# Optimization experiments

Hardware: AMD Instinct MI355X
Metric: run time of the kernel (lower is better)

Reference implementation:

```python
import math
import jax, jax.numpy as jnp
import numpy as np

NB_HEADS = 32
NB_KV_HEADS = 8
HEAD_DIM = 64
ROPE_THETA = 10000.0


def _rope_modulator(seq_len, dim, theta):
    # (seq_len, dim//2, 2): (cos, sin) of 2*pi*t / theta^(2k/d)  -- note nonstandard 2*pi factor
    freqs = 1.0 / theta ** (jnp.arange(0, dim - 1, 2, dtype=jnp.float32) / dim)
    t = jnp.arange(seq_len, dtype=jnp.float32) * (2.0 * math.pi)
    angles = t[:, None] * freqs[None, :]
    return jnp.stack((jnp.cos(angles), jnp.sin(angles)), axis=-1)


def _apply_rope(qk, rm):
    # qk: (B, H, S, hd); pairs are consecutive (even, odd) lanes
    B, H, S, hd = qk.shape
    qk = qk.reshape(B, H, S, hd // 2, 2)
    c, s = rm[:S, :, 0], rm[:S, :, 1]  # (S, hd//2)
    re = qk[..., 0] * c - qk[..., 1] * s
    im = qk[..., 0] * s + qk[..., 1] * c
    return jnp.stack((re, im), axis=-1).reshape(B, H, S, hd)


def setup_inputs() -> dict:
    key = jax.random.key(0)
    k1, k2, k3, k4, k5 = jax.random.split(key, 5)
    D = NB_HEADS * HEAD_DIM  # 2048
    Dkv = NB_KV_HEADS * HEAD_DIM  # 512
    std = D ** -0.5
    return {
        "x": jax.random.normal(k1, (2, 2048, D), dtype=jnp.float32),
        "Wq": jax.random.normal(k2, (D, D), dtype=jnp.float32) * std,
        "Wk": jax.random.normal(k3, (Dkv, D), dtype=jnp.float32) * std,
        "Wv": jax.random.normal(k4, (Dkv, D), dtype=jnp.float32) * std,
        "Wo": jax.random.normal(k5, (D, D), dtype=jnp.float32) * std,
    }


def reference(x, Wq, Wk, Wv, Wo):
    B, S, D = x.shape
    g = NB_HEADS // NB_KV_HEADS
    rm = _rope_modulator(S, HEAD_DIM, ROPE_THETA)

    q = (x @ Wq.T).reshape(B, S, NB_HEADS, HEAD_DIM).transpose(0, 2, 1, 3)
    k = (x @ Wk.T).reshape(B, S, NB_KV_HEADS, HEAD_DIM).transpose(0, 2, 1, 3)
    v = (x @ Wv.T).reshape(B, S, NB_KV_HEADS, HEAD_DIM).transpose(0, 2, 1, 3)

    q = _apply_rope(q, rm)
    k = _apply_rope(k, rm)

    # GQA: expand KV heads (repeat_interleave over head dim)
    k = jnp.repeat(k, g, axis=1)  # (B, H, S, hd)
    v = jnp.repeat(v, g, axis=1)

    scale = 1.0 / math.sqrt(HEAD_DIM)
    scores = jnp.einsum("bhqd,bhkd->bhqk", q, k) * scale
    causal = jnp.tril(jnp.ones((S, S), dtype=bool))
    scores = jnp.where(causal, scores, jnp.finfo(scores.dtype).min)
    attn = jax.nn.softmax(scores, axis=-1)
    z = jnp.einsum("bhqk,bhkd->bhqd", attn, v)  # (B, H, S, hd)
    z = z.transpose(0, 2, 1, 3).reshape(B, S, D)
    return z @ Wo.T
```

## Files before the change

### kernel.cpp

```cpp
#include <hip/hip_runtime.h>
#include <hip/hip_bf16.h>
#include <math.h>

#define B_   2
#define S_   2048
#define H_   32
#define HKV_ 8
#define HD_  64
#define D_   2048
#define DKV_ 512
#define M_   (B_*S_)

typedef __attribute__((ext_vector_type(8))) short bf16x8;
typedef __attribute__((ext_vector_type(4))) float f32x4;
typedef __attribute__((ext_vector_type(16))) float f32x16;
typedef unsigned short u16;

__device__ __forceinline__ u16 f2bf(float f) {
    union { float f; unsigned u; } v; v.f = f;
    unsigned r = v.u + 0x7fff + ((v.u >> 16) & 1);
    return (u16)(r >> 16);
}

__device__ __forceinline__ unsigned cvt_pk_bf16(float lo, float hi) {
    unsigned r;
    asm("v_cvt_pk_bf16_f32 %0, %1, %2" : "=v"(r) : "v"(lo), "v"(hi));
    return r;
}
__device__ __forceinline__ void perm32swap(unsigned &a, unsigned &b) {
    asm volatile("v_permlane32_swap_b32 %0, %1" : "+v"(a), "+v"(b));
}

typedef __attribute__((address_space(3))) void lds_void;
typedef const __attribute__((address_space(1))) void g_void;
__device__ __forceinline__ void gl_lds16(const void* g, void* l) {
    __builtin_amdgcn_global_load_lds((g_void*)g, (lds_void*)l, 16, 0, 0);
}

__global__ void rope_table_kernel(float* __restrict__ tab) {
    int idx = blockIdx.x * blockDim.x + threadIdx.x;
    int s = idx >> 5, i = idx & 31;
    double freq = pow(10000.0, -(double)i / 32.0);
    double ang = (double)s * 6.283185307179586476925286766559 * freq;
    tab[2*idx]   = (float)cos(ang);
    tab[2*idx+1] = (float)sin(ang);
}

__global__ void cvt_all_kernel(const float* __restrict__ x,  const float* __restrict__ wq,
                               const float* __restrict__ wk, const float* __restrict__ wv,
                               u16* __restrict__ xb, u16* __restrict__ wall) {
    int i = blockIdx.x * blockDim.x + threadIdx.x;
    if (i >= 1835008) return;
    const float* src; u16* dst;
    size_t e = (size_t)i * 8;
    if (i < 1048576)      { src = x  + e;            dst = xb + e; }
    else if (i < 1572864) { src = wq + (e - 8388608);  dst = wall + (e - 8388608); }
    else if (i < 1703936) { src = wk + (e - 12582912); dst = wall + 4194304 + (e - 12582912); }
    else                  { src = wv + (e - 13631488); dst = wall + 5242880 + (e - 13631488); }
    float4 a = *(const float4*)src;
    float4 b = *(const float4*)(src + 4);
    u16 tmp[8] = {f2bf(a.x), f2bf(a.y), f2bf(a.z), f2bf(a.w),
                  f2bf(b.x), f2bf(b.y), f2bf(b.z), f2bf(b.w)};
    *(uint4*)dst = *(const uint4*)tmp;
}

__global__ void cvt_bf16_kernel(const float* __restrict__ src, u16* __restrict__ dst, int n8) {
    int i = blockIdx.x * blockDim.x + threadIdx.x;
    if (i >= n8) return;
    const float4* p = (const float4*)(src + (size_t)i * 8);
    float4 a = p[0], b = p[1];
    u16 tmp[8] = {f2bf(a.x), f2bf(a.y), f2bf(a.z), f2bf(a.w),
                  f2bf(b.x), f2bf(b.y), f2bf(b.z), f2bf(b.w)};
    *(uint4*)(dst + (size_t)i * 8) = *(const uint4*)tmp;
}

template<bool YF32, bool ROPE>
__launch_bounds__(256, 2)
__global__ void gemm_bt_bf16(const u16* __restrict__ X, const u16* __restrict__ W,
                             void* __restrict__ Y, const float2* __restrict__ tab,
                             int Ndim, int Kdim) {
    __shared__ u16 As[128*32];
    __shared__ u16 Bs[128*32];
    int tid = threadIdx.x;
    int wv = tid >> 6, lane = tid & 63;
    int quad = lane >> 4, lr = lane & 15;
    int wm = wv >> 1, wn = wv & 1;
    int m0 = blockIdx.y * 128, n0 = blockIdx.x * 128;

    int srow = wv*32 + (lane >> 2);
    int scol = (lane & 3) * 8;
    const u16* xp = X + (size_t)(m0 + srow)*Kdim + scol;
    const u16* wp = W + (size_t)(n0 + srow)*Kdim + scol;

    f32x4 acc[4][4] = {};
    for (int k0 = 0; k0 < Kdim; k0 += 32) {
        __syncthreads();
        gl_lds16(xp + k0,                   &As[wv*1024]);
        gl_lds16(xp + 16*(size_t)Kdim + k0, &As[wv*1024 + 512]);
        gl_lds16(wp + k0,                   &Bs[wv*1024]);
        gl_lds16(wp + 16*(size_t)Kdim + k0, &Bs[wv*1024 + 512]);
        __syncthreads();
        bf16x8 af[4], bfr[4];
        #pragma unroll
        for (int t = 0; t < 4; ++t) {
            af[t]  = *(const bf16x8*)(&As[(wm*64 + t*16 + lr)*32 + quad*8]);
            bfr[t] = *(const bf16x8*)(&Bs[(wn*64 + t*16 + lr)*32 + quad*8]);
        }
        #pragma unroll
        for (int mt = 0; mt < 4; ++mt)
            #pragma unroll
            for (int nt = 0; nt < 4; ++nt)
                acc[mt][nt] = __builtin_amdgcn_mfma_f32_16x16x32_bf16(af[mt], bfr[nt], acc[mt][nt], 0, 0, 0);
    }
    #pragma unroll
    for (int mt = 0; mt < 4; ++mt)
        #pragma unroll
        for (int nt = 0; nt < 4; ++nt)
            #pragma unroll
            for (int r = 0; r < 4; ++r) {
                int m = m0 + wm*64 + mt*16 + quad*4 + r;
                int n = n0 + wn*64 + nt*16 + lr;
                float val = acc[mt][nt][r];
                if constexpr (ROPE) {
                    float partner = __shfl_xor(val, 1);
                    if (n < 2560) {
                        float2 cs = tab[(size_t)(m & (S_-1))*32 + ((n >> 1) & 31)];
                        val = fmaf(cs.x, val, ((n & 1) ? cs.y : -cs.y) * partner);
                    }
                }
                if constexpr (YF32)
                    ((float*)Y)[(size_t)m*Ndim + n] = val;
                else
                    ((u16*)Y)[(size_t)m*Ndim + n] = f2bf(val);
            }
}

#define LDK 40
template<bool F32>
__device__ __forceinline__ void stage8(const void* src, u16* dst, size_t row, int col, int ld) {
    if constexpr (F32) {
        const float* p = (const float*)src + row * (size_t)ld + col;
        float4 a = *(const float4*)p;
        float4 b = *(const float4*)(p + 4);
        u16 tmp[8] = {f2bf(a.x), f2bf(a.y), f2bf(a.z), f2bf(a.w),
                      f2bf(b.x), f2bf(b.y), f2bf(b.z), f2bf(b.w)};
        *(uint4*)dst = *(const uint4*)tmp;
    } else {
        const u16* p = (const u16*)src + row * (size_t)ld + col;
        *(uint4*)dst = *(const uint4*)p;
    }
}

template<bool XF32, bool WF32, bool YF32, bool ROPE>
__launch_bounds__(256, 2)
__global__ void gemm_bt(const void* __restrict__ X, const void* __restrict__ W,
                        void* __restrict__ Y, const float2* __restrict__ tab,
                        int Ndim, int Kdim) {
    __shared__ u16 As[128*LDK];
    __shared__ u16 Bs[128*LDK];
    int tid = threadIdx.x;
    int wv = tid >> 6, lane = tid & 63;
    int quad = lane >> 4, lr = lane & 15;
    int wm = wv >> 1, wn = wv & 1;
    int m0 = blockIdx.y * 128, n0 = blockIdx.x * 128;

    f32x4 acc[4][4] = {};
    for (int k0 = 0; k0 < Kdim; k0 += 32) {
        __syncthreads();
        #pragma unroll
        for (int it = 0; it < 2; ++it) {
            int e = (it*256 + tid) * 8;
            int r = e >> 5, kk = e & 31;
            stage8<XF32>(X, &As[r*LDK + kk], (size_t)(m0 + r), k0 + kk, Kdim);
            stage8<WF32>(W, &Bs[r*LDK + kk], (size_t)(n0 + r), k0 + kk, Kdim);
        }
        __syncthreads();
        bf16x8 af[4], bfr[4];
        #pragma unroll
        for (int t = 0; t < 4; ++t) {
            af[t]  = *(const bf16x8*)(&As[(wm*64 + t*16 + lr)*LDK + quad*8]);
            bfr[t] = *(const bf16x8*)(&Bs[(wn*64 + t*16 + lr)*LDK + quad*8]);
        }
        #pragma unroll
        for (int mt = 0; mt < 4; ++mt)
            #pragma unroll
            for (int nt = 0; nt < 4; ++nt)
                acc[mt][nt] = __builtin_amdgcn_mfma_f32_16x16x32_bf16(af[mt], bfr[nt], acc[mt][nt], 0, 0, 0);
    }
    #pragma unroll
    for (int mt = 0; mt < 4; ++mt)
        #pragma unroll
        for (int nt = 0; nt < 4; ++nt)
            #pragma unroll
            for (int r = 0; r < 4; ++r) {
                int m = m0 + wm*64 + mt*16 + quad*4 + r;
                int n = n0 + wn*64 + nt*16 + lr;
                float val = acc[mt][nt][r];
                if constexpr (ROPE) {
                    float partner = __shfl_xor(val, 1);
                    if (n < 2560) {
                        float2 cs = tab[(size_t)(m & (S_-1))*32 + ((n >> 1) & 31)];
                        val = fmaf(cs.x, val, ((n & 1) ? cs.y : -cs.y) * partner);
                    }
                }
                if constexpr (YF32)
                    ((float*)Y)[(size_t)m*Ndim + n] = val;
                else
                    ((u16*)Y)[(size_t)m*Ndim + n] = f2bf(val);
            }
}

__launch_bounds__(256, 4)
__global__ void attn_kernel(const u16* __restrict__ qkv, u16* __restrict__ z) {
    __shared__ u16 Ks[2][64*64];
    __shared__ u16 Vt[2][64*64];
    int tid = threadIdx.x;
    int wv = tid >> 6, lane = tid & 63;
    int qcol = lane & 31, hi = lane >> 5;
    int id = blockIdx.x;
    int qt = 15 - (id >> 6);
    int bh = id & 63;
    int h = bh >> 1, b = bh & 1;
    int kvh = h >> 2;
    int qrow_base = qt*128 + wv*32;
    int jmax = 2*qt + 1;

    const u16* qkvb = qkv + (size_t)(b*S_) * 3072;
    const u16* kbase = qkvb + 2048 + kvh*64;

    int kr = lane >> 3;
    int dcs = lane & 7;
    int sg = tid & 7;
    int sp = tid >> 3;
    const u16* vbase = qkvb + 2560 + kvh*64 + sg*8;

    #pragma unroll
    for (int i = 0; i < 2; ++i) {
        int c = 2*wv + i;
        int kvloc = c*8 + kr;
        int dc = dcs ^ ((kvloc + (kvloc >> 3)) & 7);
        gl_lds16(kbase + (size_t)kvloc*3072 + dc*8, &Ks[0][c*512]);
    }
    uint4 vr0 = *(const uint4*)(vbase + (size_t)(2*sp)*3072);
    uint4 vr1 = *(const uint4*)(vbase + (size_t)(2*sp + 1)*3072);

    bf16x8 bq[4];
    {
        const u16* qp = qkvb + (size_t)(qrow_base + qcol)*3072 + h*64 + hi*8;
        #pragma unroll
        for (int ds = 0; ds < 4; ++ds)
            bq[ds] = *(const bf16x8*)(qp + ds*16);
    }

    f32x16 oacc[2] = {};
    float lsum = 0.f;
    const float SC = 0.18033688f;

    for (int j = 0; j <= jmax; ++j) {
        int buf = j & 1;
        {
            const u16* a0 = (const u16*)&vr0;
            const u16* a1 = (const u16*)&vr1;
            #pragma unroll
            for (int jx = 0; jx < 8; ++jx) {
                unsigned pk = (unsigned)a0[jx] | ((unsigned)a1[jx] << 16);
                int kvs = (2*sp) ^ (8*(jx ^ sg));
                *(unsigned*)(&Vt[buf][(sg*8 + jx)*64 + kvs]) = pk;
            }
        }
        __syncthreads();

        if (j < jmax) {
            int kvn = (j+1)*64;
            #pragma unroll
            for (int i = 0; i < 2; ++i) {
                int c = 2*wv + i;
                int kvloc = c*8 + kr;
                int dc = dcs ^ ((kvloc + (kvloc >> 3)) & 7);
                gl_lds16(kbase + (size_t)(kvn + kvloc)*3072 + dc*8, &Ks[buf^1][c*512]);
            }
            vr0 = *(const uint4*)(vbase + (size_t)(kvn + 2*sp)*3072);
            vr1 = *(const uint4*)(vbase + (size_t)(kvn + 2*sp + 1)*3072);
        }

        int kv0 = j*64;
        if (kv0 < qrow_base + 32) {
            #pragma unroll
            for (int t = 0; t < 2; ++t) {
                int kvt = kv0 + t*32;
                if (kvt <= qrow_base + 31) {
                    f32x16 sacc = {};
                    int krow = t*32 + qcol;
                    int ksw = (krow + (krow >> 3)) & 7;
                    #pragma unroll
                    for (int ds = 0; ds < 4; ++ds) {
                        bf16x8 ak = *(const bf16x8*)(&Ks[buf][krow*64 + (((2*ds + hi) ^ ksw)*8)]);
                        sacc = __builtin_amdgcn_mfma_f32_32x32x16_bf16(ak, bq[ds], sacc, 0, 0, 0);
                    }
                    float p[16];
                    if (kvt + 31 > qrow_base) {
                        #pragma unroll
                        for (int r = 0; r < 16; ++r) {
                            int kvg = kvt + (r & 3) + 8*(r >> 2) + 4*hi;
                            float pv = exp2f(fmaf(sacc[r], SC, -4.0f));
                            if (kvg > qrow_base + qcol) pv = 0.f;
                            p[r] = pv; lsum += pv;
                        }
                    } else {
                        #pragma unroll
                        for (int r = 0; r < 16; ++r) {
                            p[r] = exp2f(fmaf(sacc[r], SC, -4.0f));
                            lsum += p[r];
                        }
                    }
                    unsigned U0[4], U1[4];
                    #pragma unroll
                    for (int g = 0; g < 4; ++g) {
                        U0[g] = cvt_pk_bf16(p[4*g],     p[4*g + 1]);
                        U1[g] = cvt_pk_bf16(p[4*g + 2], p[4*g + 3]);
                    }
                    #pragma unroll
                    for (int s = 0; s < 2; ++s) {
                        unsigned w0 = U0[2*s], w2 = U0[2*s + 1];
                        unsigned w1 = U1[2*s], w3 = U1[2*s + 1];
                        perm32swap(w0, w2);
                        perm32swap(w1, w3);
                        uint4 paw; paw.x = w0; paw.y = w1; paw.z = w2; paw.w = w3;
                        bf16x8 pa = __builtin_bit_cast(bf16x8, paw);
                        #pragma unroll
                        for (int dt = 0; dt < 2; ++dt) {
                            int d = dt*32 + qcol;
                            int g8 = (d & 7) ^ ((d >> 3) & 7);
                            int lc = 4*t + 2*s + hi;
                            bf16x8 bv = *(const bf16x8*)(&Vt[buf][d*64 + ((lc ^ g8)*8)]);
                            oacc[dt] = __builtin_amdgcn_mfma_f32_32x32x16_bf16(pa, bv, oacc[dt], 0, 0, 0);
                        }
                    }
                }
            }
        }
    }

    lsum += __shfl_xor(lsum, 32);
    __syncthreads();
    float* Lb = (float*)&Ks[0][0];
    if (hi == 0) Lb[wv*32 + qcol] = lsum;
    __syncthreads();

    #pragma unroll
    for (int r = 0; r < 16; ++r) {
        int crow = (r & 3) + 8*(r >> 2) + 4*hi;
        int row = qrow_base + crow;
        float li = Lb[wv*32 + crow];
        #pragma unroll
        for (int dt = 0; dt < 2; ++dt)
            z[(size_t)(b*S_ + row)*D_ + h*64 + dt*32 + qcol] = f2bf(oacc[dt][r] / li);
    }
}

extern "C" void kernel_launch(void* const* d_in, const int* in_sizes, int n_in,
                              void* d_out, int out_size, void* d_ws, size_t ws_size,
                              hipStream_t stream) {
    const float* x  = (const float*)d_in[0];
    const float* Wq = (const float*)d_in[1];
    const float* Wk = (const float*)d_in[2];
    const float* Wv = (const float*)d_in[3];
    const float* Wo = (const float*)d_in[4];
    float* out = (float*)d_out;
    char* ws = (char*)d_ws;

    const size_t OFF_XB   = 0;
    const size_t OFF_WALL = 16777216;
    const size_t OFF_TAB  = 29360128;
    const size_t OFF_QKV  = 29884416;
    const size_t NEED     = 55050240;

    float*  tab  = (float*)(ws + OFF_TAB);
    float2* tab2 = (float2*)(ws + OFF_TAB);

    if (ws_size >= NEED) {
        u16* xb   = (u16*)(ws + OFF_XB);
        u16* wall = (u16*)(ws + OFF_WALL);
        u16* qkv  = (u16*)(ws + OFF_QKV);
        u16* zbuf = (u16*)(ws + OFF_XB);
        u16* wob  = (u16*)(ws + 16777216);

        rope_table_kernel<<<256, 256, 0, stream>>>(tab);
        cvt_all_kernel<<<7168, 256, 0, stream>>>(x, Wq, Wk, Wv, xb, wall);
        gemm_bt_bf16<false, true><<<dim3(24, 32), 256, 0, stream>>>(xb, wall, qkv, tab2, 3072, 2048);
        cvt_bf16_kernel<<<2048, 256, 0, stream>>>(Wo, wob, D_*D_/8);
        attn_kernel<<<1024, 256, 0, stream>>>(qkv, zbuf);
        gemm_bt_bf16<true, false><<<dim3(16, 32), 256, 0, stream>>>(zbuf, wob, out, tab2, 2048, 2048);
    } else {
        u16* qkv  = (u16*)(ws + 524288);
        u16* zbuf = (u16*)(ws + 524288 + (size_t)M_*3072*2);

        rope_table_kernel<<<256, 256, 0, stream>>>(tab);
        gemm_bt<true, true, false, true ><<<dim3(16, 32), 256, 0, stream>>>(x, Wq, qkv,        tab2, 3072, 2048);
        gemm_bt<true, true, false, true ><<<dim3(4,  32), 256, 0, stream>>>(x, Wk, qkv + 2048, tab2, 3072, 2048);
        gemm_bt<true, true, false, false><<<dim3(4,  32), 256, 0, stream>>>(x, Wv, qkv + 2560, tab2, 3072, 2048);
        attn_kernel<<<1024, 256, 0, stream>>>(qkv, zbuf);
        gemm_bt<false, true, true, false><<<dim3(16, 32), 256, 0, stream>>>(zbuf, Wo, out, tab2, 2048, 2048);
    }
}
```

Measured before the change: 301.9 us.

## Use 256x256 GEMM tiles with triple-buffered async LDS pipeline

Replaces the 128x128 bf16 GEMM with a 256x256-tile, 512-thread kernel that prefetches three K-slices into LDS ahead of time. It uses explicit vmcnt waits and single barriers, so global loads overlap with the MFMA work. It also raises MFMA priority during compute. The larger tiles improve data reuse, but the grid shrinks to 192 and 128 blocks, which may underfill the 256 CUs, and triple buffering uses 96KB of LDS per block.

Measured after the change: 359.9 us. 1.19x slower.

```diff
diff --git a/kernel.cpp b/kernel.cpp
--- a/kernel.cpp
+++ b/kernel.cpp
@@ -75,50 +75,82 @@
 }
 
 template<bool YF32, bool ROPE>
-__launch_bounds__(256, 2)
-__global__ void gemm_bt_bf16(const u16* __restrict__ X, const u16* __restrict__ W,
-                             void* __restrict__ Y, const float2* __restrict__ tab,
-                             int Ndim, int Kdim) {
-    __shared__ u16 As[128*32];
-    __shared__ u16 Bs[128*32];
+__launch_bounds__(512, 2)
+__global__ void gemm_bt_256(const u16* __restrict__ X, const u16* __restrict__ W,
+                            void* __restrict__ Y, const float2* __restrict__ tab,
+                            int Ndim, int Kdim) {
+    __shared__ u16 As[3][256*32];
+    __shared__ u16 Bs[3][256*32];
     int tid = threadIdx.x;
-    int wv = tid >> 6, lane = tid & 63;
+    int wvid = tid >> 6, lane = tid & 63;
     int quad = lane >> 4, lr = lane & 15;
-    int wm = wv >> 1, wn = wv & 1;
-    int m0 = blockIdx.y * 128, n0 = blockIdx.x * 128;
-
-    int srow = wv*32 + (lane >> 2);
-    int scol = (lane & 3) * 8;
-    const u16* xp = X + (size_t)(m0 + srow)*Kdim + scol;
-    const u16* wp = W + (size_t)(n0 + srow)*Kdim + scol;
-
-    f32x4 acc[4][4] = {};
-    for (int k0 = 0; k0 < Kdim; k0 += 32) {
-        __syncthreads();
-        gl_lds16(xp + k0,                   &As[wv*1024]);
-        gl_lds16(xp + 16*(size_t)Kdim + k0, &As[wv*1024 + 512]);
-        gl_lds16(wp + k0,                   &Bs[wv*1024]);
-        gl_lds16(wp + 16*(size_t)Kdim + k0, &Bs[wv*1024 + 512]);
-        __syncthreads();
-        bf16x8 af[4], bfr[4];
-        #pragma unroll
-        for (int t = 0; t < 4; ++t) {
-            af[t]  = *(const bf16x8*)(&As[(wm*64 + t*16 + lr)*32 + quad*8]);
-            bfr[t] = *(const bf16x8*)(&Bs[(wn*64 + t*16 + lr)*32 + quad*8]);
-        }
-        #pragma unroll
-        for (int mt = 0; mt < 4; ++mt)
+    int wm = wvid >> 2, wn = wvid & 3;
+    int m0 = blockIdx.y * 256, n0 = blockIdx.x * 256;
+    const u16* Xb = X + (size_t)m0 * Kdim;
+    const u16* Wb = W + (size_t)n0 * Kdim;
+
+    int rsub = lane >> 2;
+    int cch  = (lane & 3) * 8;
+    int r0   = wvid * 32;
+    int NT   = Kdim >> 5;
+
+    #pragma unroll
+    for (int tt = 0; tt < 3; ++tt) {
+        int k0 = tt * 32;
+        #pragma unroll
+        for (int i = 0; i < 2; ++i) {
+            int br = r0 + i*16;
+            gl_lds16(Xb + (size_t)(br + rsub)*Kdim + k0 + cch, &As[tt][br*32]);
+            gl_lds16(Wb + (size_t)(br + rsub)*Kdim + k0 + cch, &Bs[tt][br*32]);
+        }
+    }
+    asm volatile("s_waitcnt vmcnt(8)" ::: "memory");
+    __builtin_amdgcn_s_barrier();
+
+    f32x4 acc[8][4] = {};
+    int slot = 0;
+    for (int t = 0; t < NT; ++t) {
+        bf16x8 af[8], bfr[4];
+        const u16* as = &As[slot][0];
+        const u16* bs = &Bs[slot][0];
+        #pragma unroll
+        for (int mt = 0; mt < 8; ++mt)
+            af[mt] = *(const bf16x8*)(as + (wm*128 + mt*16 + lr)*32 + quad*8);
+        #pragma unroll
+        for (int nt = 0; nt < 4; ++nt)
+            bfr[nt] = *(const bf16x8*)(bs + (wn*64 + nt*16 + lr)*32 + quad*8);
+        asm volatile("s_waitcnt lgkmcnt(0)" ::: "memory");
+        __builtin_amdgcn_s_barrier();
+        if (t + 3 < NT) {
+            int k0 = (t + 3) * 32;
+            #pragma unroll
+            for (int i = 0; i < 2; ++i) {
+                int br = r0 + i*16;
+                gl_lds16(Xb + (size_t)(br + rsub)*Kdim + k0 + cch, &As[slot][br*32]);
+                gl_lds16(Wb + (size_t)(br + rsub)*Kdim + k0 + cch, &Bs[slot][br*32]);
+            }
+        }
+        __builtin_amdgcn_s_setprio(1);
+        #pragma unroll
+        for (int mt = 0; mt < 8; ++mt)
             #pragma unroll
             for (int nt = 0; nt < 4; ++nt)
                 acc[mt][nt] = __builtin_amdgcn_mfma_f32_16x16x32_bf16(af[mt], bfr[nt], acc[mt][nt], 0, 0, 0);
-    }
+        __builtin_amdgcn_s_setprio(0);
+        if (t + 3 < NT)      asm volatile("s_waitcnt vmcnt(8)" ::: "memory");
+        else if (t + 2 < NT) asm volatile("s_waitcnt vmcnt(4)" ::: "memory");
+        else if (t + 1 < NT) asm volatile("s_waitcnt vmcnt(0)" ::: "memory");
+        __builtin_amdgcn_s_barrier();
+        slot = (slot == 2) ? 0 : slot + 1;
+    }
+
     #pragma unroll
-    for (int mt = 0; mt < 4; ++mt)
+    for (int mt = 0; mt < 8; ++mt)
         #pragma unroll
         for (int nt = 0; nt < 4; ++nt)
             #pragma unroll
             for (int r = 0; r < 4; ++r) {
-                int m = m0 + wm*64 + mt*16 + quad*4 + r;
+                int m = m0 + wm*128 + mt*16 + quad*4 + r;
                 int n = n0 + wn*64 + nt*16 + lr;
                 float val = acc[mt][nt][r];
                 if constexpr (ROPE) {
@@ -387,10 +419,10 @@
 
         rope_table_kernel<<<256, 256, 0, stream>>>(tab);
         cvt_all_kernel<<<7168, 256, 0, stream>>>(x, Wq, Wk, Wv, xb, wall);
-        gemm_bt_bf16<false, true><<<dim3(24, 32), 256, 0, stream>>>(xb, wall, qkv, tab2, 3072, 2048);
+        gemm_bt_256<false, true><<<dim3(12, 16), 512, 0, stream>>>(xb, wall, qkv, tab2, 3072, 2048);
         cvt_bf16_kernel<<<2048, 256, 0, stream>>>(Wo, wob, D_*D_/8);
         attn_kernel<<<1024, 256, 0, stream>>>(qkv, zbuf);
-        gemm_bt_bf16<true, false><<<dim3(16, 32), 256, 0, stream>>>(zbuf, wob, out, tab2, 2048, 2048);
+        gemm_bt_256<true, false><<<dim3(8, 16), 512, 0, stream>>>(zbuf, wob, out, tab2, 2048, 2048);
     } else {
         u16* qkv  = (u16*)(ws + 524288);
         u16* zbuf = (u16*)(ws + 524288 + (size_t)M_*3072*2);
```

## Triple-buffer bf16 GEMM LDS tiles with async prefetch and register double-buffering

Applied to the files above, without the earlier changes.

Replaces the single-buffered bf16 GEMM main loop with a three-stage LDS ring, issuing global-to-LDS loads three K-tiles ahead and waiting only on vmcnt for the oldest tile. It also preloads the next tile's fragments into registers while the MFMAs for the current tile run, and raises wave priority around the MFMA block. The aim is to hide global load latency and reduce barrier stalls in the QKV and output projections. LDS use triples, and launch bounds are raised to 3 blocks per CU, which adds register pressure and risks spills.

New measurement: 312.9 us. 3.6% more time.

```diff
diff --git a/kernel.cpp b/kernel.cpp
--- a/kernel.cpp
+++ b/kernel.cpp
@@ -75,12 +75,12 @@
 }
 
 template<bool YF32, bool ROPE>
-__launch_bounds__(256, 2)
-__global__ void gemm_bt_bf16(const u16* __restrict__ X, const u16* __restrict__ W,
-                             void* __restrict__ Y, const float2* __restrict__ tab,
-                             int Ndim, int Kdim) {
-    __shared__ u16 As[128*32];
-    __shared__ u16 Bs[128*32];
+__launch_bounds__(256, 3)
+__global__ void gemm_bt_p(const u16* __restrict__ X, const u16* __restrict__ W,
+                          void* __restrict__ Y, const float2* __restrict__ tab,
+                          int Ndim, int Kdim) {
+    __shared__ u16 As[3][128*32];
+    __shared__ u16 Bs[3][128*32];
     int tid = threadIdx.x;
     int wv = tid >> 6, lane = tid & 63;
     int quad = lane >> 4, lr = lane & 15;
@@ -91,27 +91,62 @@
     int scol = (lane & 3) * 8;
     const u16* xp = X + (size_t)(m0 + srow)*Kdim + scol;
     const u16* wp = W + (size_t)(n0 + srow)*Kdim + scol;
+    int NT = Kdim >> 5;
+
+    #pragma unroll
+    for (int tt = 0; tt < 3; ++tt) {
+        int k0 = tt << 5;
+        gl_lds16(xp + k0,                   &As[tt][wv*1024]);
+        gl_lds16(xp + 16*(size_t)Kdim + k0, &As[tt][wv*1024 + 512]);
+        gl_lds16(wp + k0,                   &Bs[tt][wv*1024]);
+        gl_lds16(wp + 16*(size_t)Kdim + k0, &Bs[tt][wv*1024 + 512]);
+    }
+    asm volatile("s_waitcnt vmcnt(8)" ::: "memory");
+    __builtin_amdgcn_s_barrier();
+
+    bf16x8 af[4], bfr[4], nf[4], nb[4];
+    #pragma unroll
+    for (int t4 = 0; t4 < 4; ++t4) {
+        af[t4]  = *(const bf16x8*)(&As[0][(wm*64 + t4*16 + lr)*32 + quad*8]);
+        bfr[t4] = *(const bf16x8*)(&Bs[0][(wn*64 + t4*16 + lr)*32 + quad*8]);
+    }
 
     f32x4 acc[4][4] = {};
-    for (int k0 = 0; k0 < Kdim; k0 += 32) {
-        __syncthreads();
-        gl_lds16(xp + k0,                   &As[wv*1024]);
-        gl_lds16(xp + 16*(size_t)Kdim + k0, &As[wv*1024 + 512]);
-        gl_lds16(wp + k0,                   &Bs[wv*1024]);
-        gl_lds16(wp + 16*(size_t)Kdim + k0, &Bs[wv*1024 + 512]);
-        __syncthreads();
-        bf16x8 af[4], bfr[4];
-        #pragma unroll
-        for (int t = 0; t < 4; ++t) {
-            af[t]  = *(const bf16x8*)(&As[(wm*64 + t*16 + lr)*32 + quad*8]);
-            bfr[t] = *(const bf16x8*)(&Bs[(wn*64 + t*16 + lr)*32 + quad*8]);
-        }
+    int slot = 0;
+    for (int t = 0; t < NT; ++t) {
+        asm volatile("s_waitcnt lgkmcnt(0)" ::: "memory");
+        __builtin_amdgcn_s_barrier();
+        if (t + 3 < NT) {
+            int k0 = (t + 3) << 5;
+            gl_lds16(xp + k0,                   &As[slot][wv*1024]);
+            gl_lds16(xp + 16*(size_t)Kdim + k0, &As[slot][wv*1024 + 512]);
+            gl_lds16(wp + k0,                   &Bs[slot][wv*1024]);
+            gl_lds16(wp + 16*(size_t)Kdim + k0, &Bs[slot][wv*1024 + 512]);
+        }
+        int slot1 = (slot == 2) ? 0 : slot + 1;
+        if (t + 1 < NT) {
+            if (t + 3 < NT)      asm volatile("s_waitcnt vmcnt(8)" ::: "memory");
+            else if (t + 2 < NT) asm volatile("s_waitcnt vmcnt(4)" ::: "memory");
+            else                 asm volatile("s_waitcnt vmcnt(0)" ::: "memory");
+            __builtin_amdgcn_s_barrier();
+            #pragma unroll
+            for (int t4 = 0; t4 < 4; ++t4) {
+                nf[t4] = *(const bf16x8*)(&As[slot1][(wm*64 + t4*16 + lr)*32 + quad*8]);
+                nb[t4] = *(const bf16x8*)(&Bs[slot1][(wn*64 + t4*16 + lr)*32 + quad*8]);
+            }
+        }
+        __builtin_amdgcn_s_setprio(1);
         #pragma unroll
         for (int mt = 0; mt < 4; ++mt)
             #pragma unroll
             for (int nt = 0; nt < 4; ++nt)
                 acc[mt][nt] = __builtin_amdgcn_mfma_f32_16x16x32_bf16(af[mt], bfr[nt], acc[mt][nt], 0, 0, 0);
-    }
+        __builtin_amdgcn_s_setprio(0);
+        #pragma unroll
+        for (int t4 = 0; t4 < 4; ++t4) { af[t4] = nf[t4]; bfr[t4] = nb[t4]; }
+        slot = slot1;
+    }
+
     #pragma unroll
     for (int mt = 0; mt < 4; ++mt)
         #pragma unroll
@@ -387,10 +422,10 @@
 
         rope_table_kernel<<<256, 256, 0, stream>>>(tab);
         cvt_all_kernel<<<7168, 256, 0, stream>>>(x, Wq, Wk, Wv, xb, wall);
-        gemm_bt_bf16<false, true><<<dim3(24, 32), 256, 0, stream>>>(xb, wall, qkv, tab2, 3072, 2048);
+        gemm_bt_p<false, true><<<dim3(24, 32), 256, 0, stream>>>(xb, wall, qkv, tab2, 3072, 2048);
         cvt_bf16_kernel<<<2048, 256, 0, stream>>>(Wo, wob, D_*D_/8);
         attn_kernel<<<1024, 256, 0, stream>>>(qkv, zbuf);
-        gemm_bt_bf16<true, false><<<dim3(16, 32), 256, 0, stream>>>(zbuf, wob, out, tab2, 2048, 2048);
+        gemm_bt_p<true, false><<<dim3(16, 32), 256, 0, stream>>>(zbuf, wob, out, tab2, 2048, 2048);
     } else {
         u16* qkv  = (u16*)(ws + 524288);
         u16* zbuf = (u16*)(ws + 524288 + (size_t)M_*3072*2);
```

## Replace bf16 GEMM with 256x256 double-buffered 8-phase pipelined kernel

Applied to the files above, without the earlier changes.

Replaces the 128x128, single-buffered bf16 GEMM with a 256x256 tile kernel using 8 waves and double-buffered LDS. It also XOR-swizzles the LDS layout and splits each K step into four phases. Each phase issues the next tile's global-to-LDS loads while running MFMAs under raised wave priority, with explicit vmcnt waits and barriers. The aim is to hide global load latency, raise data reuse per block and cut LDS bank conflicts. The cost is far fewer blocks (192 and 128) than the GPU has CUs, so part of the chip may sit idle, plus heavy LDS use per block.

Result: slower. 366.7 us (+21.4%).

```diff
diff --git a/kernel.cpp b/kernel.cpp
--- a/kernel.cpp
+++ b/kernel.cpp
@@ -74,51 +74,99 @@
     *(uint4*)(dst + (size_t)i * 8) = *(const uint4*)tmp;
 }
 
+#define GPH(BI, MH, NH, W4, STA, G0, G1, KT) do {                                          \
+    if (W4) asm volatile("s_waitcnt vmcnt(4)" ::: "memory");                               \
+    asm volatile("" ::: "memory");                                                         \
+    __builtin_amdgcn_s_barrier();                                                          \
+    asm volatile("" ::: "memory");                                                         \
+    bf16x8 af_[4][2], bf_[2][2];                                                           \
+    _Pragma("unroll")                                                                      \
+    for (int mtl = 0; mtl < 4; ++mtl)                                                      \
+        _Pragma("unroll")                                                                  \
+        for (int kk = 0; kk < 2; ++kk)                                                     \
+            af_[mtl][kk] = *(const bf16x8*)(&As[BI][(rA + ((MH)*4+mtl)*16)*64 + (((kk*4+quad)^sw)*8)]); \
+    _Pragma("unroll")                                                                      \
+    for (int ntl = 0; ntl < 2; ++ntl)                                                      \
+        _Pragma("unroll")                                                                  \
+        for (int kk = 0; kk < 2; ++kk)                                                     \
+            bf_[ntl][kk] = *(const bf16x8*)(&Bs[BI][(rB + ((NH)*2+ntl)*16)*64 + (((kk*4+quad)^sw)*8)]); \
+    { int k0s_ = (KT) << 6;                                                                \
+      if (STA) { gl_lds16(xsrc + ((size_t)((G0)*8))*Kdim + k0s_, &As[1-(BI)][(G0)*512]);   \
+                 gl_lds16(xsrc + ((size_t)((G1)*8))*Kdim + k0s_, &As[1-(BI)][(G1)*512]); } \
+      else     { gl_lds16(wsrc + ((size_t)((G0)*8))*Kdim + k0s_, &Bs[1-(BI)][(G0)*512]);   \
+                 gl_lds16(wsrc + ((size_t)((G1)*8))*Kdim + k0s_, &Bs[1-(BI)][(G1)*512]); } } \
+    asm volatile("s_waitcnt lgkmcnt(0)" ::: "memory");                                     \
+    __builtin_amdgcn_sched_barrier(0);                                                     \
+    __builtin_amdgcn_s_setprio(1);                                                         \
+    _Pragma("unroll")                                                                      \
+    for (int mtl = 0; mtl < 4; ++mtl)                                                      \
+        _Pragma("unroll")                                                                  \
+        for (int ntl = 0; ntl < 2; ++ntl) {                                                \
+            acc[(MH)*4+mtl][(NH)*2+ntl] = __builtin_amdgcn_mfma_f32_16x16x32_bf16(af_[mtl][0], bf_[ntl][0], acc[(MH)*4+mtl][(NH)*2+ntl], 0, 0, 0); \
+            acc[(MH)*4+mtl][(NH)*2+ntl] = __builtin_amdgcn_mfma_f32_16x16x32_bf16(af_[mtl][1], bf_[ntl][1], acc[(MH)*4+mtl][(NH)*2+ntl], 0, 0, 0); \
+        }                                                                                  \
+    __builtin_amdgcn_s_setprio(0);                                                         \
+} while (0)
+
 template<bool YF32, bool ROPE>
-__launch_bounds__(256, 2)
-__global__ void gemm_bt_bf16(const u16* __restrict__ X, const u16* __restrict__ W,
-                             void* __restrict__ Y, const float2* __restrict__ tab,
-                             int Ndim, int Kdim) {
-    __shared__ u16 As[128*32];
-    __shared__ u16 Bs[128*32];
+__launch_bounds__(512, 2)
+__global__ void gemm_bt_8p(const u16* __restrict__ X, const u16* __restrict__ W,
+                           void* __restrict__ Y, const float2* __restrict__ tab,
+                           int Ndim, int Kdim) {
+    __shared__ u16 As[2][256*64];
+    __shared__ u16 Bs[2][256*64];
     int tid = threadIdx.x;
-    int wv = tid >> 6, lane = tid & 63;
+    int wvid = tid >> 6, lane = tid & 63;
     int quad = lane >> 4, lr = lane & 15;
-    int wm = wv >> 1, wn = wv & 1;
-    int m0 = blockIdx.y * 128, n0 = blockIdx.x * 128;
-
-    int srow = wv*32 + (lane >> 2);
-    int scol = (lane & 3) * 8;
-    const u16* xp = X + (size_t)(m0 + srow)*Kdim + scol;
-    const u16* wp = W + (size_t)(n0 + srow)*Kdim + scol;
-
-    f32x4 acc[4][4] = {};
-    for (int k0 = 0; k0 < Kdim; k0 += 32) {
-        __syncthreads();
-        gl_lds16(xp + k0,                   &As[wv*1024]);
-        gl_lds16(xp + 16*(size_t)Kdim + k0, &As[wv*1024 + 512]);
-        gl_lds16(wp + k0,                   &Bs[wv*1024]);
-        gl_lds16(wp + 16*(size_t)Kdim + k0, &Bs[wv*1024 + 512]);
-        __syncthreads();
-        bf16x8 af[4], bfr[4];
-        #pragma unroll
-        for (int t = 0; t < 4; ++t) {
-            af[t]  = *(const bf16x8*)(&As[(wm*64 + t*16 + lr)*32 + quad*8]);
-            bfr[t] = *(const bf16x8*)(&Bs[(wn*64 + t*16 + lr)*32 + quad*8]);
-        }
-        #pragma unroll
-        for (int mt = 0; mt < 4; ++mt)
-            #pragma unroll
-            for (int nt = 0; nt < 4; ++nt)
-                acc[mt][nt] = __builtin_amdgcn_mfma_f32_16x16x32_bf16(af[mt], bfr[nt], acc[mt][nt], 0, 0, 0);
-    }
+    int wm = wvid >> 2, wn = wvid & 3;
+    int m0 = blockIdx.y * 256, n0 = blockIdx.x * 256;
+    int sw = lr & 7;
+    int rA = wm*128 + lr;
+    int rB = wn*64 + lr;
+
+    int lgr = lane >> 3, lch = lane & 7;
+    size_t goff = (size_t)lgr * Kdim + (size_t)((lch ^ lgr) * 8);
+    const u16* xsrc = X + (size_t)m0 * Kdim + goff;
+    const u16* wsrc = W + (size_t)n0 * Kdim + goff;
+
+    int c0 = wvid*2, c1 = wvid*2 + 1;
+    int gA0 = (c0>>3)*16 + (c0&7),     gA1 = (c1>>3)*16 + (c1&7);
+    int gA2 = (c0>>3)*16 + 8 + (c0&7), gA3 = (c1>>3)*16 + 8 + (c1&7);
+    int gB0 = (c0>>2)*8 + (c0&3),      gB1 = (c1>>2)*8 + (c1&3);
+    int gB2 = (c0>>2)*8 + 4 + (c0&3),  gB3 = (c1>>2)*8 + 4 + (c1&3);
+
+    int NT64 = Kdim >> 6;
+
+    gl_lds16(xsrc + ((size_t)(gA0*8))*Kdim, &As[0][gA0*512]);
+    gl_lds16(xsrc + ((size_t)(gA1*8))*Kdim, &As[0][gA1*512]);
+    gl_lds16(wsrc + ((size_t)(gB0*8))*Kdim, &Bs[0][gB0*512]);
+    gl_lds16(wsrc + ((size_t)(gB1*8))*Kdim, &Bs[0][gB1*512]);
+    gl_lds16(wsrc + ((size_t)(gB2*8))*Kdim, &Bs[0][gB2*512]);
+    gl_lds16(wsrc + ((size_t)(gB3*8))*Kdim, &Bs[0][gB3*512]);
+    gl_lds16(xsrc + ((size_t)(gA2*8))*Kdim, &As[0][gA2*512]);
+    gl_lds16(xsrc + ((size_t)(gA3*8))*Kdim, &As[0][gA3*512]);
+
+    f32x4 acc[8][4] = {};
+    for (int t = 0; t < (NT64 >> 1); ++t) {
+        int kt1 = 2*t + 1;
+        int kt2 = (2*t + 2 < NT64) ? (2*t + 2) : 0;
+        GPH(0, 0, 0, 1, 1, gA0, gA1, kt1);
+        GPH(0, 0, 1, 1, 0, gB0, gB1, kt1);
+        GPH(0, 1, 0, 1, 0, gB2, gB3, kt1);
+        GPH(0, 1, 1, 0, 1, gA2, gA3, kt1);
+        GPH(1, 0, 0, 1, 1, gA0, gA1, kt2);
+        GPH(1, 0, 1, 1, 0, gB0, gB1, kt2);
+        GPH(1, 1, 0, 1, 0, gB2, gB3, kt2);
+        GPH(1, 1, 1, 0, 1, gA2, gA3, kt2);
+    }
+
     #pragma unroll
-    for (int mt = 0; mt < 4; ++mt)
+    for (int mt = 0; mt < 8; ++mt)
         #pragma unroll
         for (int nt = 0; nt < 4; ++nt)
             #pragma unroll
             for (int r = 0; r < 4; ++r) {
-                int m = m0 + wm*64 + mt*16 + quad*4 + r;
+                int m = m0 + wm*128 + mt*16 + quad*4 + r;
                 int n = n0 + wn*64 + nt*16 + lr;
                 float val = acc[mt][nt][r];
                 if constexpr (ROPE) {
@@ -387,10 +435,10 @@
 
         rope_table_kernel<<<256, 256, 0, stream>>>(tab);
         cvt_all_kernel<<<7168, 256, 0, stream>>>(x, Wq, Wk, Wv, xb, wall);
-        gemm_bt_bf16<false, true><<<dim3(24, 32), 256, 0, stream>>>(xb, wall, qkv, tab2, 3072, 2048);
+        gemm_bt_8p<false, true><<<dim3(12, 16), 512, 0, stream>>>(xb, wall, qkv, tab2, 3072, 2048);
         cvt_bf16_kernel<<<2048, 256, 0, stream>>>(Wo, wob, D_*D_/8);
         attn_kernel<<<1024, 256, 0, stream>>>(qkv, zbuf);
-        gemm_bt_bf16<true, false><<<dim3(16, 32), 256, 0, stream>>>(zbuf, wob, out, tab2, 2048, 2048);
+        gemm_bt_8p<true, false><<<dim3(8, 16), 512, 0, stream>>>(zbuf, wob, out, tab2, 2048, 2048);
     } else {
         u16* qkv  = (u16*)(ws + 524288);
         u16* zbuf = (u16*)(ws + 524288 + (size_t)M_*3072*2);
```
